# Kernel optimization log

Hardware: AMD Instinct MI355X
Metric: run time of the kernel (lower is better)

## Reference

```python
import jax, jax.numpy as jnp
import numpy as np

VOCAB, EMBED, HIDDEN = 32000, 512, 1024
B, T = 2, 2048
LN_EPS = 1e-5


def setup_inputs() -> dict:
    key = jax.random.key(0)
    ks = jax.random.split(key, 12)

    def xavier(k, fan_in, fan_out):
        lim = float(np.sqrt(6.0 / (fan_in + fan_out)))
        return jax.random.uniform(k, (fan_in, fan_out), jnp.float32, -lim, lim)

    return {
        "tokens": jax.random.randint(ks[0], (B, T), 0, VOCAB),
        "E": xavier(ks[1], VOCAB, EMBED),                    # embedding table
        "Wc": xavier(ks[2], EMBED, HIDDEN),                  # fc_current (stored [in,out])
        "bc": jnp.full((HIDDEN,), 0.01, jnp.float32),
        "Wh": xavier(ks[3], EMBED, HIDDEN),                  # fc_context
        "bh": jnp.full((HIDDEN,), 0.01, jnp.float32),
        "Wm": xavier(ks[4], 2 * HIDDEN, HIDDEN),             # fc_merge
        "bm": jnp.full((HIDDEN,), 0.01, jnp.float32),
        "Wo": xavier(ks[5], HIDDEN, VOCAB),                  # fc_out
        "bo": jnp.full((VOCAB,), 0.01, jnp.float32),
        "ln_w": jnp.ones((HIDDEN,), jnp.float32),
        "ln_b": jnp.zeros((HIDDEN,), jnp.float32),
    }


def reference(tokens, E, Wc, bc, Wh, bh, Wm, bm, Wo, bo, ln_w, ln_b):
    emb = E[tokens]  # [B, T, D]
    # history mean at step t = mean(emb[:, :t]); at t==0 the module uses current embed
    csum = jnp.cumsum(emb, axis=1)
    counts = jnp.arange(1, T, dtype=emb.dtype)[None, :, None]
    hist_mean = jnp.concatenate([emb[:, :1], csum[:, :-1] / counts], axis=1)  # [B,T,D]

    cur_enc = jax.nn.relu(jnp.einsum("btd,dh->bth", emb, Wc) + bc)
    hist_enc = jax.nn.relu(jnp.einsum("btd,dh->bth", hist_mean, Wh) + bh)
    merged = jnp.concatenate([cur_enc, hist_enc], axis=-1)  # [B,T,2H]
    merged = jax.nn.relu(jnp.einsum("btk,kh->bth", merged, Wm) + bm)

    mu = jnp.mean(merged, axis=-1, keepdims=True)
    var = jnp.mean(jnp.square(merged - mu), axis=-1, keepdims=True)
    normed = (merged - mu) * jax.lax.rsqrt(var + LN_EPS) * ln_w + ln_b

    logits = (jnp.einsum("bth,hv->btv", normed, Wo) + bo) / 10.0  # [B,T,V]
    return logits
```

## Files before the change

kernel.cpp:

```cpp
#include <hip/hip_runtime.h>
#include <hip/hip_bf16.h>
#include <stdint.h>
#include <stdio.h>

#define T_SEQ  2048
#define BATCH  2
#define NROWS  4096
#define EMBED  512
#define HIDDEN 1024
#define VOCAB  32000
#define NCHUNK 128
#define CHLEN  16

typedef __bf16 bf16x8 __attribute__((ext_vector_type(8)));
typedef float  f32x4  __attribute__((ext_vector_type(4)));

__device__ __forceinline__ float b2f(unsigned short h) {
  union { unsigned int u; float f; } v; v.u = ((unsigned int)h) << 16; return v.f;
}
__device__ __forceinline__ unsigned short f2b(float f) {
  union { float f; unsigned int u; } v; v.f = f;
  unsigned int u = v.u;
  u += 0x7fffu + ((u >> 16) & 1u);
  return (unsigned short)(u >> 16);
}

__global__ void gather_sum_kernel(const int* __restrict__ tokens,
                                  const float* __restrict__ E,
                                  unsigned short* __restrict__ emb,
                                  float* __restrict__ csum) {
  const int bc = blockIdx.x;
  const int d  = threadIdx.x;
  __shared__ int tok[CHLEN];
  if (d < CHLEN) tok[d] = tokens[bc * CHLEN + d];
  __syncthreads();
  float s = 0.f;
  unsigned short* eo = emb + ((size_t)bc * CHLEN) * EMBED + d;
  #pragma unroll 4
  for (int i = 0; i < CHLEN; ++i) {
    const float v = E[(size_t)tok[i] * EMBED + d];
    const unsigned short h = f2b(v);
    eo[(size_t)i * EMBED] = h;
    s += b2f(h);
  }
  csum[(size_t)bc * EMBED + d] = s;
}

__global__ void scan_excl_kernel(float* __restrict__ csum) {
  const int b  = blockIdx.x;
  const int d0 = blockIdx.y << 7;
  const int t  = threadIdx.x;
  __shared__ float s[NCHUNK][128];
  for (int c = 0; c < NCHUNK; ++c)
    s[c][t] = csum[((size_t)b * NCHUNK + c) * EMBED + d0 + t];
  float run = 0.f;
  for (int c = 0; c < NCHUNK; ++c) {
    const float v = s[c][t];
    csum[((size_t)b * NCHUNK + c) * EMBED + d0 + t] = run;
    run += v;
  }
}

__global__ void scan_emit_kernel(const unsigned short* __restrict__ emb,
                                 const float* __restrict__ csum,
                                 unsigned short* __restrict__ hist) {
  const int bc = blockIdx.x;
  const int c  = bc & (NCHUNK - 1);
  const int d  = threadIdx.x;
  const unsigned short* e = emb  + ((size_t)bc * CHLEN) * EMBED + d;
  unsigned short*       h = hist + ((size_t)bc * CHLEN) * EMBED + d;
  float sum = csum[(size_t)bc * EMBED + d];
  #pragma unroll 8
  for (int i = 0; i < CHLEN; ++i) {
    const int t = c * CHLEN + i;
    h[(size_t)i * EMBED] = (t == 0) ? e[0] : f2b(sum / (float)t);
    sum += b2f(e[(size_t)i * EMBED]);
  }
}

__global__ __launch_bounds__(256) void transpose_all_kernel(
    const float* __restrict__ Wc, const float* __restrict__ Wh,
    const float* __restrict__ Wm, const float* __restrict__ Wo,
    unsigned short* __restrict__ WcT, unsigned short* __restrict__ WhT,
    unsigned short* __restrict__ WmT, unsigned short* __restrict__ WoT) {
  const int id = blockIdx.x;
  const float* in; unsigned short* out; int R, C, t;
  if (id < 128)      { in = Wc; out = WcT; R = 512;  C = 1024;  t = id; }
  else if (id < 256) { in = Wh; out = WhT; R = 512;  C = 1024;  t = id - 128; }
  else if (id < 768) { in = Wm; out = WmT; R = 2048; C = 1024;  t = id - 256; }
  else               { in = Wo; out = WoT; R = 1024; C = 32000; t = id - 768; }
  const int tilesX = C >> 6;
  const int r0 = (t / tilesX) << 6, c0 = (t % tilesX) << 6;

  __shared__ float tile[64][65];
  const int tid = threadIdx.x;
  #pragma unroll
  for (int p = 0; p < 4; ++p) {
    const int u = tid + p * 256;
    const int row = u >> 4, cq = (u & 15) << 2;
    const float4 v = *(const float4*)&in[(size_t)(r0 + row) * C + c0 + cq];
    tile[row][cq + 0] = v.x; tile[row][cq + 1] = v.y;
    tile[row][cq + 2] = v.z; tile[row][cq + 3] = v.w;
  }
  __syncthreads();
  #pragma unroll
  for (int p = 0; p < 4; ++p) {
    const int u = tid + p * 256;
    const int oc = u >> 4, org = (u & 15) << 2;
    ushort4 o;
    o.x = f2b(tile[org + 0][oc]); o.y = f2b(tile[org + 1][oc]);
    o.z = f2b(tile[org + 2][oc]); o.w = f2b(tile[org + 3][oc]);
    *(ushort4*)&out[(size_t)(c0 + oc) * R + r0 + org] = o;
  }
}

__device__ __forceinline__ void async16(unsigned short* lds, const unsigned short* g) {
  __builtin_amdgcn_global_load_lds(
      (const __attribute__((address_space(1))) void*)g,
      (__attribute__((address_space(3))) void*)lds, 16, 0, 0);
}

#define BM 128
#define BN 128
#define BK 32

template<int MODE>
__global__ __launch_bounds__(256) void gemm_bt_kernel(
    const unsigned short* __restrict__ A,
    const unsigned short* __restrict__ BT,
    const float* __restrict__ bias,
    void* __restrict__ out, int M, int N, int K, int ldOut, int colOff,
    const unsigned short* __restrict__ A2,
    const unsigned short* __restrict__ BT2,
    const float* __restrict__ bias2, int colOff2) {
  __shared__ unsigned short As[BM * BK];
  __shared__ unsigned short Bs[BN * BK];

  const unsigned short* Ap = A;
  const unsigned short* Bp = BT;
  const float*          bp = bias;
  int                   co = colOff;
  if (blockIdx.z) { Ap = A2; Bp = BT2; bp = bias2; co = colOff2; }

  int wg = blockIdx.x;
  {
    const int nwg = gridDim.x;
    const int xcd = wg & 7, loc = wg >> 3;
    const int q = nwg >> 3, r = nwg & 7;
    wg = (xcd < r ? xcd * (q + 1) : r * (q + 1) + (xcd - r) * q) + loc;
  }
  const int nmb = M / BM;
  const int mb  = wg % nmb;
  const int nb  = wg / nmb;
  const int m0  = mb * BM;
  const int n0  = nb * BN;

  const int tid  = threadIdx.x;
  const int wave = tid >> 6;
  const int lane = tid & 63;
  const int wm = (wave & 1) * 64;
  const int wn = (wave >> 1) * 64;

  const int srow = (wave << 5) + (lane >> 2);
  const int scol = (lane & 3) << 3;
  const unsigned short* aSrc = Ap + (size_t)(m0 + srow) * K + scol;
  const unsigned short* bSrc = Bp + (size_t)(n0 + srow) * K + scol;
  unsigned short* aDst = As + (wave << 5) * BK;
  unsigned short* bDst = Bs + (wave << 5) * BK;

  f32x4 acc[4][4];
  #pragma unroll
  for (int i = 0; i < 4; ++i)
    #pragma unroll
    for (int j = 0; j < 4; ++j)
      acc[i][j] = (f32x4){0.f, 0.f, 0.f, 0.f};

  const int q = lane >> 4;
  const int r = lane & 15;

  for (int k0 = 0; k0 < K; k0 += BK) {
    __syncthreads();
    async16(aDst,           aSrc);
    async16(aDst + 16 * BK, aSrc + 16 * (size_t)K);
    async16(bDst,           bSrc);
    async16(bDst + 16 * BK, bSrc + 16 * (size_t)K);
    aSrc += BK; bSrc += BK;
    __syncthreads();

    bf16x8 af[4], bfr[4];
    #pragma unroll
    for (int mi = 0; mi < 4; ++mi)
      af[mi] = *(const bf16x8*)&As[(wm + mi * 16 + r) * BK + (q << 3)];
    #pragma unroll
    for (int ni = 0; ni < 4; ++ni)
      bfr[ni] = *(const bf16x8*)&Bs[(wn + ni * 16 + r) * BK + (q << 3)];
    #pragma unroll
    for (int mi = 0; mi < 4; ++mi)
      #pragma unroll
      for (int ni = 0; ni < 4; ++ni)
        acc[mi][ni] = __builtin_amdgcn_mfma_f32_16x16x32_bf16(
            af[mi], bfr[ni], acc[mi][ni], 0, 0, 0);
  }

  #pragma unroll
  for (int ni = 0; ni < 4; ++ni) {
    const int col = n0 + wn + ni * 16 + r;
    const float bv = bp[col];
    #pragma unroll
    for (int mi = 0; mi < 4; ++mi) {
      #pragma unroll
      for (int e = 0; e < 4; ++e) {
        const int row = m0 + wm + mi * 16 + (q << 2) + e;
        float v = fmaxf(acc[mi][ni][e] + bv, 0.f);
        const size_t idx = (size_t)row * ldOut + co + col;
        if (MODE == 0) ((unsigned short*)out)[idx] = f2b(v);
        else           ((float*)out)[idx] = v;
      }
    }
  }
}


#define BAR() do {                            \
    asm volatile("" ::: "memory");            \
    __builtin_amdgcn_sched_barrier(0);        \
    __builtin_amdgcn_s_barrier();             \
    __builtin_amdgcn_sched_barrier(0);        \
    asm volatile("" ::: "memory");            \
  } while (0)

__global__ __launch_bounds__(512, 2) void gemm256_out_kernel(
    const unsigned short* __restrict__ A,
    const unsigned short* __restrict__ BT,
    const float* __restrict__ bias,
    float* __restrict__ out, int M, int N, int K, int ldOut) {
  __shared__ unsigned short lds[2][2][2][8192];

  int wg = blockIdx.x;
  {
    const int nwg = gridDim.x;
    const int xcd = wg & 7, loc = wg >> 3;
    const int q8 = nwg >> 3, r8 = nwg & 7;
    wg = (xcd < r8 ? xcd * (q8 + 1) : r8 * (q8 + 1) + (xcd - r8) * q8) + loc;
  }
  const int nmb = M >> 8;
  const int mb = wg % nmb, nb = wg / nmb;
  const int m0 = mb << 8, n0 = nb << 8;

  const int tid  = threadIdx.x;
  const int wave = tid >> 6, lane = tid & 63;
  const int wr = wave >> 2, wc = wave & 3;
  const int q = lane >> 4, r = lane & 15, rr = lane & 7;

  const int srow = (wave << 4) + (lane >> 3);
  const int scol = ((lane & 7) ^ (lane >> 3)) << 3;
  const unsigned short* aB = A  + (size_t)(m0 + srow) * K + scol;
  const unsigned short* bB = BT + (size_t)(n0 + srow) * K + scol;

  const int NTt = K >> 6;

  auto stage = [&](int matB, int h, int tb, int kt) {
    unsigned short* d = &lds[tb][matB][h][wave << 10];
    const unsigned short* s =
        (matB ? bB : aB) + (size_t)h * 128 * K + ((size_t)kt << 6);
    async16(d, s);
    async16(d + 512, s + ((size_t)K << 3));
  };

  auto ldA = [&](int tb, int mi, int ks) {
    return *(const bf16x8*)&lds[tb][0][wr]
        [(mi * 16 + r) * 64 + ((((ks << 2) | q) ^ rr) << 3)];
  };
  auto ldB = [&](int tb, int ni, int ks) {
    return *(const bf16x8*)&lds[tb][1][wc >> 1]
        [(((wc & 1) << 6) + ni * 16 + r) * 64 + ((((ks << 2) | q) ^ rr) << 3)];
  };

  f32x4 acc[8][4];
  #pragma unroll
  for (int i = 0; i < 8; ++i)
    #pragma unroll
    for (int j = 0; j < 4; ++j)
      acc[i][j] = (f32x4){0.f, 0.f, 0.f, 0.f};

  bf16x8 afr[8][2], bfr[2][2];

  stage(0, 0, 0, 0); stage(0, 1, 0, 0); stage(1, 0, 0, 0); stage(1, 1, 0, 0);
  if (NTt > 1) {
    stage(0, 0, 1, 1); stage(0, 1, 1, 1); stage(1, 0, 1, 1);
    asm volatile("s_waitcnt vmcnt(6)" ::: "memory");
  } else {
    asm volatile("s_waitcnt vmcnt(0)" ::: "memory");
  }
  BAR();

#define TILE(U, BU) do {                                                       \
    const int u_ = (U);                                                        \
                            \
    _Pragma("unroll")                                                          \
    for (int mi = 0; mi < 4; ++mi) {                                           \
      afr[mi][0] = ldA(BU, mi, 0); afr[mi][1] = ldA(BU, mi, 1);                \
    }                                                                          \
    _Pragma("unroll")                                                          \
    for (int nj = 0; nj < 2; ++nj) {                                           \
      bfr[nj][0] = ldB(BU, nj, 0); bfr[nj][1] = ldB(BU, nj, 1);                \
    }                                                                          \
    if (u_ + 1 < NTt) stage(1, 1, 1 - (BU), u_ + 1);                           \
    __builtin_amdgcn_s_setprio(1);                                             \
    _Pragma("unroll")                                                          \
    for (int mi = 0; mi < 4; ++mi)                                             \
      _Pragma("unroll")                                                        \
      for (int nj = 0; nj < 2; ++nj) {                                         \
        acc[mi][nj] = __builtin_amdgcn_mfma_f32_16x16x32_bf16(                 \
            afr[mi][0], bfr[nj][0], acc[mi][nj], 0, 0, 0);                     \
        acc[mi][nj] = __builtin_amdgcn_mfma_f32_16x16x32_bf16(                 \
            afr[mi][1], bfr[nj][1], acc[mi][nj], 0, 0, 0);                     \
      }                                                                        \
    __builtin_amdgcn_s_setprio(0);                                             \
    BAR();                                                                     \
                                 \
    _Pragma("unroll")                                                          \
    for (int mi = 4; mi < 8; ++mi) {                                           \
      afr[mi][0] = ldA(BU, mi, 0); afr[mi][1] = ldA(BU, mi, 1);                \
    }                                                                          \
    __builtin_amdgcn_s_setprio(1);                                             \
    _Pragma("unroll")                                                          \
    for (int mi = 4; mi < 8; ++mi)                                             \
      _Pragma("unroll")                                                        \
      for (int nj = 0; nj < 2; ++nj) {                                         \
        acc[mi][nj] = __builtin_amdgcn_mfma_f32_16x16x32_bf16(                 \
            afr[mi][0], bfr[nj][0], acc[mi][nj], 0, 0, 0);                     \
        acc[mi][nj] = __builtin_amdgcn_mfma_f32_16x16x32_bf16(                 \
            afr[mi][1], bfr[nj][1], acc[mi][nj], 0, 0, 0);                     \
      }                                                                        \
    __builtin_amdgcn_s_setprio(0);                                             \
    BAR();                                                                     \
                            \
    _Pragma("unroll")                                                          \
    for (int nj = 0; nj < 2; ++nj) {                                           \
      bfr[nj][0] = ldB(BU, 2 + nj, 0); bfr[nj][1] = ldB(BU, 2 + nj, 1);        \
    }                                                                          \
    if (u_ + 2 < NTt) stage(0, 0, BU, u_ + 2);                                 \
    __builtin_amdgcn_s_setprio(1);                                             \
    _Pragma("unroll")                                                          \
    for (int mi = 0; mi < 4; ++mi)                                             \
      _Pragma("unroll")                                                        \
      for (int nj = 0; nj < 2; ++nj) {                                         \
        acc[mi][2 + nj] = __builtin_amdgcn_mfma_f32_16x16x32_bf16(             \
            afr[mi][0], bfr[nj][0], acc[mi][2 + nj], 0, 0, 0);                 \
        acc[mi][2 + nj] = __builtin_amdgcn_mfma_f32_16x16x32_bf16(             \
            afr[mi][1], bfr[nj][1], acc[mi][2 + nj], 0, 0, 0);                 \
      }                                                                        \
    __builtin_amdgcn_s_setprio(0);                                             \
    BAR();                                                                     \
                   \
    if (u_ + 2 < NTt) { stage(0, 1, BU, u_ + 2); stage(1, 0, BU, u_ + 2); }    \
    __builtin_amdgcn_s_setprio(1);                                             \
    _Pragma("unroll")                                                          \
    for (int mi = 4; mi < 8; ++mi)                                             \
      _Pragma("unroll")                                                        \
      for (int nj = 0; nj < 2; ++nj) {                                         \
        acc[mi][2 + nj] = __builtin_amdgcn_mfma_f32_16x16x32_bf16(             \
            afr[mi][0], bfr[nj][0], acc[mi][2 + nj], 0, 0, 0);                 \
        acc[mi][2 + nj] = __builtin_amdgcn_mfma_f32_16x16x32_bf16(             \
            afr[mi][1], bfr[nj][1], acc[mi][2 + nj], 0, 0, 0);                 \
      }                                                                        \
    __builtin_amdgcn_s_setprio(0);                                             \
    if (u_ + 2 < NTt) asm volatile("s_waitcnt vmcnt(6)" ::: "memory");         \
    else              asm volatile("s_waitcnt vmcnt(0)" ::: "memory");         \
    BAR();                                                                     \
  } while (0)

  for (int u = 0; u < NTt; u += 2) {
    TILE(u, 0);
    TILE(u + 1, 1);
  }
#undef TILE

  float* scratch = (float*)&lds[0][0][0][0];
  #pragma unroll
  for (int p = 0; p < 2; ++p) {
    if (wr == p) {
      #pragma unroll
      for (int ni = 0; ni < 4; ++ni) {
        const int col = (wc << 6) + ni * 16 + r;
        const float bv = bias[n0 + col];
        #pragma unroll
        for (int mi = 0; mi < 8; ++mi) {
          #pragma unroll
          for (int e = 0; e < 4; ++e) {
            const int row = mi * 16 + (q << 2) + e;
            const int cs  = col ^ (((row >> 2) & 1) << 4);
            scratch[row * 256 + cs] = (acc[mi][ni][e] + bv) * 0.1f;
          }
        }
      }
    }
    __syncthreads();
    #pragma unroll
    for (int rowi = 0; rowi < 16; ++rowi) {
      const int row = (wave << 4) + rowi;
      const int cb  = (lane << 2) ^ (((row >> 2) & 1) << 4);
      const f32x4 v4 = *(const f32x4*)&scratch[row * 256 + cb];
      __builtin_nontemporal_store(
          v4, (f32x4*)&out[(size_t)(m0 + (p << 7) + row) * ldOut + n0 + (lane << 2)]);
    }
    __syncthreads();
  }
}

__global__ void ln_kernel(const float* __restrict__ merged,
                          const float* __restrict__ lnw,
                          const float* __restrict__ lnb,
                          unsigned short* __restrict__ normed) {
  const int row = blockIdx.x;
  const float4 v = ((const float4*)(merged + (size_t)row * HIDDEN))[threadIdx.x];
  float s  = v.x + v.y + v.z + v.w;
  float ss = v.x * v.x + v.y * v.y + v.z * v.z + v.w * v.w;
  #pragma unroll
  for (int off = 32; off > 0; off >>= 1) {
    s  += __shfl_down(s, off, 64);
    ss += __shfl_down(ss, off, 64);
  }
  __shared__ float red[8];
  const int wvi = threadIdx.x >> 6;
  if ((threadIdx.x & 63) == 0) { red[wvi] = s; red[4 + wvi] = ss; }
  __syncthreads();
  s  = red[0] + red[1] + red[2] + red[3];
  ss = red[4] + red[5] + red[6] + red[7];
  const float mu  = s * (1.0f / HIDDEN);
  const float var = ss * (1.0f / HIDDEN) - mu * mu;
  const float rs  = rsqrtf(var + 1e-5f);
  const float4 w4 = ((const float4*)lnw)[threadIdx.x];
  const float4 b4 = ((const float4*)lnb)[threadIdx.x];
  ushort4 o;
  o.x = f2b((v.x - mu) * rs * w4.x + b4.x);
  o.y = f2b((v.y - mu) * rs * w4.y + b4.y);
  o.z = f2b((v.z - mu) * rs * w4.z + b4.z);
  o.w = f2b((v.w - mu) * rs * w4.w + b4.w);
  ((ushort4*)(normed + (size_t)row * HIDDEN))[threadIdx.x] = o;
}

extern "C" void kernel_launch(void* const* d_in, const int* in_sizes, int n_in,
                              void* d_out, int out_size, void* d_ws, size_t ws_size,
                              hipStream_t stream) {
  const int*   tokens = (const int*)d_in[0];
  const float* E      = (const float*)d_in[1];
  const float* Wc     = (const float*)d_in[2];
  const float* bc     = (const float*)d_in[3];
  const float* Wh     = (const float*)d_in[4];
  const float* bh     = (const float*)d_in[5];
  const float* Wm     = (const float*)d_in[6];
  const float* bm     = (const float*)d_in[7];
  const float* Wo     = (const float*)d_in[8];
  const float* bo     = (const float*)d_in[9];
  const float* lnw    = (const float*)d_in[10];
  const float* lnb    = (const float*)d_in[11];

  char* p = (char*)d_ws;
  unsigned short* WcT  = (unsigned short*)p; p += (size_t)HIDDEN * EMBED * 2;
  unsigned short* WhT  = (unsigned short*)p; p += (size_t)HIDDEN * EMBED * 2;
  unsigned short* WmT  = (unsigned short*)p; p += (size_t)HIDDEN * (2 * HIDDEN) * 2;
  unsigned short* WoT  = (unsigned short*)p; p += (size_t)VOCAB * HIDDEN * 2;
  unsigned short* emb  = (unsigned short*)p; p += (size_t)NROWS * EMBED * 2;
  unsigned short* hist = (unsigned short*)p; p += (size_t)NROWS * EMBED * 2;
  unsigned short* cat  = (unsigned short*)p; p += (size_t)NROWS * (2 * HIDDEN) * 2;
  float*          mrg  = (float*)p;          p += (size_t)NROWS * HIDDEN * 4;
  unsigned short* nrm  = (unsigned short*)p; p += (size_t)NROWS * HIDDEN * 2;
  float*          csum = (float*)p;          p += (size_t)BATCH * NCHUNK * EMBED * 4;
  if ((size_t)(p - (char*)d_ws) > ws_size)
    fprintf(stderr, "WS TOO SMALL: need %zu have %zu\n", (size_t)(p - (char*)d_ws), ws_size);

  transpose_all_kernel<<<8768, 256, 0, stream>>>(Wc, Wh, Wm, Wo, WcT, WhT, WmT, WoT);

  gather_sum_kernel<<<BATCH * NCHUNK, EMBED, 0, stream>>>(tokens, E, emb, csum);
  scan_excl_kernel<<<dim3(BATCH, EMBED / 128), 128, 0, stream>>>(csum);
  scan_emit_kernel<<<BATCH * NCHUNK, EMBED, 0, stream>>>(emb, csum, hist);

  const int nwgEnc = (NROWS / BM) * (HIDDEN / BN);

  gemm_bt_kernel<0><<<dim3(nwgEnc, 1, 2), 256, 0, stream>>>(
      emb, WcT, bc, cat, NROWS, HIDDEN, EMBED, 2 * HIDDEN, 0,
      hist, WhT, bh, HIDDEN);
  gemm_bt_kernel<1><<<dim3(nwgEnc, 1, 1), 256, 0, stream>>>(
      cat, WmT, bm, mrg, NROWS, HIDDEN, 2 * HIDDEN, HIDDEN, 0,
      nullptr, nullptr, nullptr, 0);
  ln_kernel<<<NROWS, 256, 0, stream>>>(mrg, lnw, lnb, nrm);

  const int nwgOut = (NROWS / 256) * (VOCAB / 256);
  gemm256_out_kernel<<<dim3(nwgOut), 512, 0, stream>>>(
      nrm, WoT, bo, (float*)d_out, NROWS, VOCAB, HIDDEN, VOCAB);
}
```

Before: 941.1 us.

## Double-buffer LDS in encoder GEMM and fuse transpose with embedding gather

The encoder/merge GEMM now uses two LDS buffers and issues the next K-tile's async loads before computing on the current tile, with a single barrier per iteration instead of two. The weight transpose and the embedding gather/chunk-sum are merged into one launch with 512-thread blocks, which saves a kernel launch and lets the two jobs run concurrently. The cost is doubled LDS use per GEMM block, which may lower occupancy. Correctness relies on the barrier waiting for the async LDS loads.

Result: no change. 939.9 us (median of 2 runs) (-0.1%).

```diff
diff --git a/kernel.cpp b/kernel.cpp
--- a/kernel.cpp
+++ b/kernel.cpp
@@ -25,25 +25,68 @@
   return (unsigned short)(u >> 16);
 }
 
-__global__ void gather_sum_kernel(const int* __restrict__ tokens,
-                                  const float* __restrict__ E,
-                                  unsigned short* __restrict__ emb,
-                                  float* __restrict__ csum) {
-  const int bc = blockIdx.x;
-  const int d  = threadIdx.x;
-  __shared__ int tok[CHLEN];
-  if (d < CHLEN) tok[d] = tokens[bc * CHLEN + d];
+__device__ __forceinline__ void async16(unsigned short* lds, const unsigned short* g) {
+  __builtin_amdgcn_global_load_lds(
+      (const __attribute__((address_space(1))) void*)g,
+      (__attribute__((address_space(3))) void*)lds, 16, 0, 0);
+}
+
+__global__ __launch_bounds__(512) void prep_kernel(
+    const int* __restrict__ tokens, const float* __restrict__ E,
+    unsigned short* __restrict__ emb, float* __restrict__ csum,
+    const float* __restrict__ Wc, const float* __restrict__ Wh,
+    const float* __restrict__ Wm, const float* __restrict__ Wo,
+    unsigned short* __restrict__ WcT, unsigned short* __restrict__ WhT,
+    unsigned short* __restrict__ WmT, unsigned short* __restrict__ WoT) {
+  const int id = blockIdx.x;
+
+  if (id >= 8768) {
+    const int bc = id - 8768;
+    const int d  = threadIdx.x;
+    __shared__ int tok[CHLEN];
+    if (d < CHLEN) tok[d] = tokens[bc * CHLEN + d];
+    __syncthreads();
+    float s = 0.f;
+    unsigned short* eo = emb + ((size_t)bc * CHLEN) * EMBED + d;
+    #pragma unroll 4
+    for (int i = 0; i < CHLEN; ++i) {
+      const float v = E[(size_t)tok[i] * EMBED + d];
+      const unsigned short h = f2b(v);
+      eo[(size_t)i * EMBED] = h;
+      s += b2f(h);
+    }
+    csum[(size_t)bc * EMBED + d] = s;
+    return;
+  }
+
+  const float* in; unsigned short* out; int R, C, t;
+  if (id < 128)      { in = Wc; out = WcT; R = 512;  C = 1024;  t = id; }
+  else if (id < 256) { in = Wh; out = WhT; R = 512;  C = 1024;  t = id - 128; }
+  else if (id < 768) { in = Wm; out = WmT; R = 2048; C = 1024;  t = id - 256; }
+  else               { in = Wo; out = WoT; R = 1024; C = 32000; t = id - 768; }
+  const int tilesX = C >> 6;
+  const int r0 = (t / tilesX) << 6, c0 = (t % tilesX) << 6;
+
+  __shared__ float tile[64][65];
+  const int tid = threadIdx.x;
+  #pragma unroll
+  for (int p = 0; p < 2; ++p) {
+    const int u = tid + p * 512;
+    const int row = u >> 4, cq = (u & 15) << 2;
+    const float4 v = *(const float4*)&in[(size_t)(r0 + row) * C + c0 + cq];
+    tile[row][cq + 0] = v.x; tile[row][cq + 1] = v.y;
+    tile[row][cq + 2] = v.z; tile[row][cq + 3] = v.w;
+  }
   __syncthreads();
-  float s = 0.f;
-  unsigned short* eo = emb + ((size_t)bc * CHLEN) * EMBED + d;
-  #pragma unroll 4
-  for (int i = 0; i < CHLEN; ++i) {
-    const float v = E[(size_t)tok[i] * EMBED + d];
-    const unsigned short h = f2b(v);
-    eo[(size_t)i * EMBED] = h;
-    s += b2f(h);
-  }
-  csum[(size_t)bc * EMBED + d] = s;
+  #pragma unroll
+  for (int p = 0; p < 2; ++p) {
+    const int u = tid + p * 512;
+    const int oc = u >> 4, org = (u & 15) << 2;
+    ushort4 o;
+    o.x = f2b(tile[org + 0][oc]); o.y = f2b(tile[org + 1][oc]);
+    o.z = f2b(tile[org + 2][oc]); o.w = f2b(tile[org + 3][oc]);
+    *(ushort4*)&out[(size_t)(c0 + oc) * R + r0 + org] = o;
+  }
 }
 
 __global__ void scan_excl_kernel(float* __restrict__ csum) {
@@ -78,48 +121,6 @@
   }
 }
 
-__global__ __launch_bounds__(256) void transpose_all_kernel(
-    const float* __restrict__ Wc, const float* __restrict__ Wh,
-    const float* __restrict__ Wm, const float* __restrict__ Wo,
-    unsigned short* __restrict__ WcT, unsigned short* __restrict__ WhT,
-    unsigned short* __restrict__ WmT, unsigned short* __restrict__ WoT) {
-  const int id = blockIdx.x;
-  const float* in; unsigned short* out; int R, C, t;
-  if (id < 128)      { in = Wc; out = WcT; R = 512;  C = 1024;  t = id; }
-  else if (id < 256) { in = Wh; out = WhT; R = 512;  C = 1024;  t = id - 128; }
-  else if (id < 768) { in = Wm; out = WmT; R = 2048; C = 1024;  t = id - 256; }
-  else               { in = Wo; out = WoT; R = 1024; C = 32000; t = id - 768; }
-  const int tilesX = C >> 6;
-  const int r0 = (t / tilesX) << 6, c0 = (t % tilesX) << 6;
-
-  __shared__ float tile[64][65];
-  const int tid = threadIdx.x;
-  #pragma unroll
-  for (int p = 0; p < 4; ++p) {
-    const int u = tid + p * 256;
-    const int row = u >> 4, cq = (u & 15) << 2;
-    const float4 v = *(const float4*)&in[(size_t)(r0 + row) * C + c0 + cq];
-    tile[row][cq + 0] = v.x; tile[row][cq + 1] = v.y;
-    tile[row][cq + 2] = v.z; tile[row][cq + 3] = v.w;
-  }
-  __syncthreads();
-  #pragma unroll
-  for (int p = 0; p < 4; ++p) {
-    const int u = tid + p * 256;
-    const int oc = u >> 4, org = (u & 15) << 2;
-    ushort4 o;
-    o.x = f2b(tile[org + 0][oc]); o.y = f2b(tile[org + 1][oc]);
-    o.z = f2b(tile[org + 2][oc]); o.w = f2b(tile[org + 3][oc]);
-    *(ushort4*)&out[(size_t)(c0 + oc) * R + r0 + org] = o;
-  }
-}
-
-__device__ __forceinline__ void async16(unsigned short* lds, const unsigned short* g) {
-  __builtin_amdgcn_global_load_lds(
-      (const __attribute__((address_space(1))) void*)g,
-      (__attribute__((address_space(3))) void*)lds, 16, 0, 0);
-}
-
 #define BM 128
 #define BN 128
 #define BK 32
@@ -133,8 +134,8 @@
     const unsigned short* __restrict__ A2,
     const unsigned short* __restrict__ BT2,
     const float* __restrict__ bias2, int colOff2) {
-  __shared__ unsigned short As[BM * BK];
-  __shared__ unsigned short Bs[BN * BK];
+  __shared__ unsigned short As[2][BM * BK];
+  __shared__ unsigned short Bs[2][BN * BK];
 
   const unsigned short* Ap = A;
   const unsigned short* Bp = BT;
@@ -165,8 +166,7 @@
   const int scol = (lane & 3) << 3;
   const unsigned short* aSrc = Ap + (size_t)(m0 + srow) * K + scol;
   const unsigned short* bSrc = Bp + (size_t)(n0 + srow) * K + scol;
-  unsigned short* aDst = As + (wave << 5) * BK;
-  unsigned short* bDst = Bs + (wave << 5) * BK;
+  const int ldsOff = (wave << 5) * BK;
 
   f32x4 acc[4][4];
   #pragma unroll
@@ -178,28 +178,37 @@
   const int q = lane >> 4;
   const int r = lane & 15;
 
-  for (int k0 = 0; k0 < K; k0 += BK) {
-    __syncthreads();
-    async16(aDst,           aSrc);
-    async16(aDst + 16 * BK, aSrc + 16 * (size_t)K);
-    async16(bDst,           bSrc);
-    async16(bDst + 16 * BK, bSrc + 16 * (size_t)K);
+  auto stageT = [&](int buf) {
+    async16(&As[buf][ldsOff],           aSrc);
+    async16(&As[buf][ldsOff + 16 * BK], aSrc + 16 * (size_t)K);
+    async16(&Bs[buf][ldsOff],           bSrc);
+    async16(&Bs[buf][ldsOff + 16 * BK], bSrc + 16 * (size_t)K);
     aSrc += BK; bSrc += BK;
-    __syncthreads();
+  };
+
+  const int nt = K / BK;
+  stageT(0);
+  __syncthreads();
+
+  for (int t = 0; t < nt; ++t) {
+    const int c = t & 1;
+    if (t + 1 < nt) stageT(1 - c);
 
     bf16x8 af[4], bfr[4];
     #pragma unroll
     for (int mi = 0; mi < 4; ++mi)
-      af[mi] = *(const bf16x8*)&As[(wm + mi * 16 + r) * BK + (q << 3)];
+      af[mi] = *(const bf16x8*)&As[c][(wm + mi * 16 + r) * BK + (q << 3)];
     #pragma unroll
     for (int ni = 0; ni < 4; ++ni)
-      bfr[ni] = *(const bf16x8*)&Bs[(wn + ni * 16 + r) * BK + (q << 3)];
+      bfr[ni] = *(const bf16x8*)&Bs[c][(wn + ni * 16 + r) * BK + (q << 3)];
     #pragma unroll
     for (int mi = 0; mi < 4; ++mi)
       #pragma unroll
       for (int ni = 0; ni < 4; ++ni)
         acc[mi][ni] = __builtin_amdgcn_mfma_f32_16x16x32_bf16(
             af[mi], bfr[ni], acc[mi][ni], 0, 0, 0);
+
+    __syncthreads();
   }
 
   #pragma unroll
@@ -471,9 +480,8 @@
   if ((size_t)(p - (char*)d_ws) > ws_size)
     fprintf(stderr, "WS TOO SMALL: need %zu have %zu\n", (size_t)(p - (char*)d_ws), ws_size);
 
-  transpose_all_kernel<<<8768, 256, 0, stream>>>(Wc, Wh, Wm, Wo, WcT, WhT, WmT, WoT);
-
-  gather_sum_kernel<<<BATCH * NCHUNK, EMBED, 0, stream>>>(tokens, E, emb, csum);
+  prep_kernel<<<8768 + 256, 512, 0, stream>>>(
+      tokens, E, emb, csum, Wc, Wh, Wm, Wo, WcT, WhT, WmT, WoT);
   scan_excl_kernel<<<dim3(BATCH, EMBED / 128), 128, 0, stream>>>(csum);
   scan_emit_kernel<<<BATCH * NCHUNK, EMBED, 0, stream>>>(emb, csum, hist);
 
```
